# Performance work log

Measured on AMD Instinct MI355X. Metric: run time of the kernel, lower is better.

## Reference

```python
import jax, jax.numpy as jnp
import numpy as np

H = 1024
NH = 16
HD = H // NH
EPS = 1e-5


def setup_inputs() -> dict:
    key = jax.random.key(0)
    ks = jax.random.split(key, 16)
    B, LQ, LK = 2, 1024, 2048
    s = 1.0 / np.sqrt(H)
    inp = {
        "query": jax.random.normal(ks[0], (B, LQ, H), jnp.float32),
        "key": jax.random.normal(ks[1], (B, LK, H), jnp.float32),
        "value": jax.random.normal(ks[2], (B, LK, H), jnp.float32),
        "mask": jax.random.randint(ks[3], (B, LQ, LK), 0, 2, jnp.int32),
        "Wq": jax.random.normal(ks[4], (H, H), jnp.float32) * s,
        "bq": jnp.zeros((H,), jnp.float32),
        "Wk": jax.random.normal(ks[5], (H, H), jnp.float32) * s,
        "bk": jnp.zeros((H,), jnp.float32),
        "Wv": jax.random.normal(ks[6], (H, H), jnp.float32) * s,
        "bv": jnp.zeros((H,), jnp.float32),
        "Wo": jax.random.normal(ks[7], (H, H), jnp.float32) * s,
        "bo": jnp.zeros((H,), jnp.float32),
        "ln_g": jnp.ones((H,), jnp.float32),
        "ln_b": jnp.zeros((H,), jnp.float32),
    }
    return inp


def _split_heads(x, B, L):
    # [B, L, H] -> [B, NH, L, HD]
    return x.reshape(B, L, NH, HD).transpose(0, 2, 1, 3)


def reference(query, key, value, mask, Wq, bq, Wk, bk, Wv, bv, Wo, bo, ln_g, ln_b):
    B, LQ, _ = query.shape
    LK = key.shape[1]
    # projections (torch Linear: x @ W.T + b)
    Q = _split_heads(query @ Wq.T + bq, B, LQ)   # [B,NH,LQ,HD]
    K = _split_heads(key   @ Wk.T + bk, B, LK)   # [B,NH,LK,HD]
    V = _split_heads(value @ Wv.T + bv, B, LK)   # [B,NH,LK,HD]
    scores = jnp.einsum('bhqd,bhkd->bhqk', Q, K) / np.sqrt(HD)
    scores = jnp.where(mask[:, None, :, :] == 0, jnp.float32(-1e9), scores)
    attn = jax.nn.softmax(scores, axis=-1)
    # dropout is identity in eval mode
    ctx = jnp.einsum('bhqk,bhkd->bhqd', attn, V)            # [B,NH,LQ,HD]
    ctx = ctx.transpose(0, 2, 1, 3).reshape(B, LQ, H)       # [B,LQ,H]
    out = ctx @ Wo.T + bo
    x = out + query
    mu = jnp.mean(x, axis=-1, keepdims=True)
    var = jnp.mean(jnp.square(x - mu), axis=-1, keepdims=True)
    return (x - mu) / jnp.sqrt(var + EPS) * ln_g + ln_b
```

## Files before the change

### kernel.cpp

```cpp
#include <hip/hip_runtime.h>
#include <hip/hip_bf16.h>

typedef __hip_bfloat16 hbf16;

#define Hdim 1024
#define NHEAD 16
#define HDIM 64
#define BATCH 2
#define LQ 1024
#define LK 2048
#define LN_EPS 1e-5f

typedef __bf16 bfv8 __attribute__((ext_vector_type(8)));
typedef float floatx4 __attribute__((ext_vector_type(4)));
typedef union { bfv8 v; unsigned short s[8]; } bfu8;

#define GP 72

__device__ inline bfv8 cvt2(const float4 x, const float4 y) {
    bfv8 r = {(__bf16)x.x, (__bf16)x.y, (__bf16)x.z, (__bf16)x.w,
              (__bf16)y.x, (__bf16)y.y, (__bf16)y.z, (__bf16)y.w};
    return r;
}

__global__ __launch_bounds__(256, 2) void proj_qkv(
    const float* __restrict__ query, const float* __restrict__ key,
    const float* __restrict__ value,
    const float* __restrict__ Wq, const float* __restrict__ bq,
    const float* __restrict__ Wk, const float* __restrict__ bk,
    const float* __restrict__ Wv, const float* __restrict__ bv,
    hbf16* __restrict__ Qp, hbf16* __restrict__ Kp, hbf16* __restrict__ Vp) {
    const int z = blockIdx.z;
    if (z == 0 && blockIdx.y >= (BATCH * LQ) / 128) return;

    const float* A; const float* W; const float* bias; hbf16* out;
    if (z == 0)      { A = query; W = Wq; bias = bq; out = Qp; }
    else if (z == 1) { A = key;   W = Wk; bias = bk; out = Kp; }
    else             { A = value; W = Wv; bias = bv; out = Vp; }

    __shared__ __align__(16) __bf16 As[128 * GP];
    __shared__ __align__(16) __bf16 Bs[128 * GP];
    const int tid = threadIdx.x;
    const int lane = tid & 63;
    const int w = tid >> 6;
    const int wm = w & 1, wn = w >> 1;
    const int u = lane & 15, quad = lane >> 4;
    const int rowBase = blockIdx.y * 128;
    const int colBase = blockIdx.x * 128;
    const int srow = tid >> 3;
    const int scol = (tid & 7) * 8;

    floatx4 acc[4][4] = {};

    for (int k0 = 0; k0 < Hdim; k0 += 64) {
        bfv8 av[4], bv8[4];
#pragma unroll
        for (int p = 0; p < 4; ++p) {
            const float* ap = A + (size_t)(rowBase + p * 32 + srow) * Hdim + k0 + scol;
            av[p] = cvt2(((const float4*)ap)[0], ((const float4*)ap)[1]);
            const float* wp = W + (size_t)(colBase + p * 32 + srow) * Hdim + k0 + scol;
            bv8[p] = cvt2(((const float4*)wp)[0], ((const float4*)wp)[1]);
        }
        __syncthreads();
#pragma unroll
        for (int p = 0; p < 4; ++p) {
            *(bfv8*)&As[(p * 32 + srow) * GP + scol] = av[p];
            *(bfv8*)&Bs[(p * 32 + srow) * GP + scol] = bv8[p];
        }
        __syncthreads();
#pragma unroll
        for (int ks = 0; ks < 64; ks += 32) {
            bfv8 af[4], bf[4];
#pragma unroll
            for (int i = 0; i < 4; ++i) {
                af[i] = *(const bfv8*)&As[(wm * 64 + i * 16 + u) * GP + ks + quad * 8];
                bf[i] = *(const bfv8*)&Bs[(wn * 64 + i * 16 + u) * GP + ks + quad * 8];
            }
#pragma unroll
            for (int mt = 0; mt < 4; ++mt)
#pragma unroll
                for (int nt = 0; nt < 4; ++nt)
                    acc[mt][nt] = __builtin_amdgcn_mfma_f32_16x16x32_bf16(af[mt], bf[nt], acc[mt][nt], 0, 0, 0);
        }
    }

#pragma unroll
    for (int nt = 0; nt < 4; ++nt) {
        const int n = colBase + wn * 64 + nt * 16 + u;
        const float bn = bias[n];
#pragma unroll
        for (int mt = 0; mt < 4; ++mt)
#pragma unroll
            for (int rr = 0; rr < 4; ++rr) {
                const int m = rowBase + wm * 64 + mt * 16 + quad * 4 + rr;
                out[(size_t)m * Hdim + n] = __float2bfloat16(acc[mt][nt][rr] + bn);
            }
    }
}

__global__ __launch_bounds__(256, 2) void gemm_ctx128(const hbf16* __restrict__ A,
                                                      const float* __restrict__ W,
                                                      const float* __restrict__ bias,
                                                      const float* __restrict__ resid,
                                                      float* __restrict__ out) {
    __shared__ __align__(16) __bf16 As[128 * GP];
    __shared__ __align__(16) __bf16 Bs[128 * GP];
    const int tid = threadIdx.x;
    const int lane = tid & 63;
    const int w = tid >> 6;
    const int wm = w & 1, wn = w >> 1;
    const int u = lane & 15, quad = lane >> 4;
    const int rowBase = blockIdx.y * 128;
    const int colBase = blockIdx.x * 128;
    const int srow = tid >> 3;
    const int scol = (tid & 7) * 8;

    floatx4 acc[4][4] = {};

    for (int k0 = 0; k0 < Hdim; k0 += 64) {
        bfv8 av[4], bv8[4];
#pragma unroll
        for (int p = 0; p < 4; ++p) {
            av[p] = *(const bfv8*)(A + (size_t)(rowBase + p * 32 + srow) * Hdim + k0 + scol);
            const float* wp = W + (size_t)(colBase + p * 32 + srow) * Hdim + k0 + scol;
            bv8[p] = cvt2(((const float4*)wp)[0], ((const float4*)wp)[1]);
        }
        __syncthreads();
#pragma unroll
        for (int p = 0; p < 4; ++p) {
            *(bfv8*)&As[(p * 32 + srow) * GP + scol] = av[p];
            *(bfv8*)&Bs[(p * 32 + srow) * GP + scol] = bv8[p];
        }
        __syncthreads();
#pragma unroll
        for (int ks = 0; ks < 64; ks += 32) {
            bfv8 af[4], bf[4];
#pragma unroll
            for (int i = 0; i < 4; ++i) {
                af[i] = *(const bfv8*)&As[(wm * 64 + i * 16 + u) * GP + ks + quad * 8];
                bf[i] = *(const bfv8*)&Bs[(wn * 64 + i * 16 + u) * GP + ks + quad * 8];
            }
#pragma unroll
            for (int mt = 0; mt < 4; ++mt)
#pragma unroll
                for (int nt = 0; nt < 4; ++nt)
                    acc[mt][nt] = __builtin_amdgcn_mfma_f32_16x16x32_bf16(af[mt], bf[nt], acc[mt][nt], 0, 0, 0);
        }
    }

#pragma unroll
    for (int nt = 0; nt < 4; ++nt) {
        const int n = colBase + wn * 64 + nt * 16 + u;
        const float bn = bias[n];
#pragma unroll
        for (int mt = 0; mt < 4; ++mt)
#pragma unroll
            for (int rr = 0; rr < 4; ++rr) {
                const int m = rowBase + wm * 64 + mt * 16 + quad * 4 + rr;
                out[(size_t)m * Hdim + n] = acc[mt][nt][rr] + bn + resid[(size_t)m * Hdim + n];
            }
    }
}

#define QT 64
#define KT 64
#define KS_PITCH 72
#define VT_OFF(d) ((d) * 72 + (((d) >> 3) << 3))
#define PS_OFF(r) ((r) * 72 + (((r) >> 2) << 3))

__global__ __launch_bounds__(256, 4) void attn_flash(const hbf16* __restrict__ Qp,
                                                     const hbf16* __restrict__ Kp,
                                                     const hbf16* __restrict__ Vp,
                                                     const int* __restrict__ mask,
                                                     hbf16* __restrict__ ctx) {
    const int qb = blockIdx.x;
    const int h = blockIdx.y;
    const int b = blockIdx.z;
    const int tid = threadIdx.x;
    const int lane = tid & 63;
    const int w = tid >> 6;
    const int u = lane & 15;
    const int quad = lane >> 4;
    const int qBase = qb * QT;

    __shared__ __align__(16) __bf16 Ks[64 * KS_PITCH];
    __shared__ __align__(16) __bf16 Vt[4672];
    __shared__ __align__(16) __bf16 Ps[4][1184];

    const int qrow_frag = qBase + w * 16 + u;
    const hbf16* qptr = Qp + (size_t)(b * LQ + qrow_frag) * Hdim + h * HDIM + quad * 8;
    const bfv8 af_q0 = *(const bfv8*)qptr;
    const bfv8 af_q1 = *(const bfv8*)(qptr + 32);

    float m_run[4], l_run[4];
    floatx4 acc_o[4];
#pragma unroll
    for (int r = 0; r < 4; ++r) { m_run[r] = -1e30f; l_run[r] = 0.f; }
#pragma unroll
    for (int nd = 0; nd < 4; ++nd) acc_o[nd] = (floatx4){0.f, 0.f, 0.f, 0.f};

    const int sk = tid >> 2;
    const int sdg = (tid & 3) * 16;
    const int vk2 = (tid >> 3) * 2;
    const int vd0 = (tid & 7) * 8;
    const int* mbase = mask + ((size_t)(b * LQ + qBase + w * 16 + quad * 4)) * LK + u;

    for (int kt = 0; kt < LK / KT; ++kt) {
        const int kBase = kt * KT;

        int mv[4][4];
#pragma unroll
        for (int ns = 0; ns < 4; ++ns)
#pragma unroll
            for (int rr = 0; rr < 4; ++rr)
                mv[ns][rr] = mbase[(size_t)rr * LK + kBase + ns * 16];

        const hbf16* vp0 = Vp + (size_t)(b * LK + kBase + vk2) * Hdim + h * HDIM + vd0;
        bfu8 v0, v1;
        v0.v = *(const bfv8*)vp0;
        v1.v = *(const bfv8*)(vp0 + Hdim);
        const hbf16* kp = Kp + (size_t)(b * LK + kBase + sk) * Hdim + h * HDIM + sdg;
        const bfv8 kv0 = *(const bfv8*)kp;
        const bfv8 kv1 = *(const bfv8*)(kp + 8);

        __syncthreads();
        *(bfv8*)&Ks[sk * KS_PITCH + sdg] = kv0;
        *(bfv8*)&Ks[sk * KS_PITCH + sdg + 8] = kv1;
#pragma unroll
        for (int i = 0; i < 8; ++i) {
            unsigned int pk = (unsigned int)v0.s[i] | ((unsigned int)v1.s[i] << 16);
            *(unsigned int*)&Vt[VT_OFF(vd0 + i) + vk2] = pk;
        }
        __syncthreads();

        floatx4 acc_s[4];
#pragma unroll
        for (int ns = 0; ns < 4; ++ns) {
            const bfv8 bk0 = *(const bfv8*)&Ks[(ns * 16 + u) * KS_PITCH + quad * 8];
            const bfv8 bk1 = *(const bfv8*)&Ks[(ns * 16 + u) * KS_PITCH + quad * 8 + 32];
            floatx4 a = (floatx4){0.f, 0.f, 0.f, 0.f};
            a = __builtin_amdgcn_mfma_f32_16x16x32_bf16(af_q0, bk0, a, 0, 0, 0);
            a = __builtin_amdgcn_mfma_f32_16x16x32_bf16(af_q1, bk1, a, 0, 0, 0);
            acc_s[ns] = a;
        }

        float pvv[4][4];
#pragma unroll
        for (int ns = 0; ns < 4; ++ns)
#pragma unroll
            for (int rr = 0; rr < 4; ++rr) {
                float s = acc_s[ns][rr] * 0.125f;
                if (mv[ns][rr] == 0) s = -1e9f;
                pvv[ns][rr] = s;
            }

        float alpha[4];
#pragma unroll
        for (int rr = 0; rr < 4; ++rr) {
            float tmax = fmaxf(fmaxf(pvv[0][rr], pvv[1][rr]), fmaxf(pvv[2][rr], pvv[3][rr]));
            tmax = fmaxf(tmax, __shfl_xor(tmax, 1, 64));
            tmax = fmaxf(tmax, __shfl_xor(tmax, 2, 64));
            tmax = fmaxf(tmax, __shfl_xor(tmax, 4, 64));
            tmax = fmaxf(tmax, __shfl_xor(tmax, 8, 64));
            const float mn = fmaxf(m_run[rr], tmax);
            alpha[rr] = __expf(m_run[rr] - mn);
            m_run[rr] = mn;
            float tsum = 0.f;
#pragma unroll
            for (int ns = 0; ns < 4; ++ns) {
                const float e = __expf(pvv[ns][rr] - mn);
                pvv[ns][rr] = e;
                tsum += e;
            }
            tsum += __shfl_xor(tsum, 1, 64);
            tsum += __shfl_xor(tsum, 2, 64);
            tsum += __shfl_xor(tsum, 4, 64);
            tsum += __shfl_xor(tsum, 8, 64);
            l_run[rr] = l_run[rr] * alpha[rr] + tsum;
        }

        __bf16* Pw = Ps[w];
#pragma unroll
        for (int ns = 0; ns < 4; ++ns)
#pragma unroll
            for (int rr = 0; rr < 4; ++rr)
                Pw[PS_OFF(quad * 4 + rr) + ns * 16 + u] = (__bf16)pvv[ns][rr];
#pragma unroll
        for (int nd = 0; nd < 4; ++nd)
#pragma unroll
            for (int rr = 0; rr < 4; ++rr)
                acc_o[nd][rr] *= alpha[rr];

        const bfv8 af_p0 = *(const bfv8*)&Pw[PS_OFF(u) + quad * 8];
        const bfv8 af_p1 = *(const bfv8*)&Pw[PS_OFF(u) + quad * 8 + 32];
#pragma unroll
        for (int nd = 0; nd < 4; ++nd) {
            const bfv8 bv0 = *(const bfv8*)&Vt[VT_OFF(nd * 16 + u) + quad * 8];
            const bfv8 bv1 = *(const bfv8*)&Vt[VT_OFF(nd * 16 + u) + quad * 8 + 32];
            acc_o[nd] = __builtin_amdgcn_mfma_f32_16x16x32_bf16(af_p0, bv0, acc_o[nd], 0, 0, 0);
            acc_o[nd] = __builtin_amdgcn_mfma_f32_16x16x32_bf16(af_p1, bv1, acc_o[nd], 0, 0, 0);
        }
    }

#pragma unroll
    for (int rr = 0; rr < 4; ++rr) {
        const float invl = 1.0f / l_run[rr];
        const int qrow = qBase + w * 16 + quad * 4 + rr;
        hbf16* crow = ctx + (size_t)(b * LQ + qrow) * Hdim + h * HDIM;
#pragma unroll
        for (int nd = 0; nd < 4; ++nd)
            crow[nd * 16 + u] = __float2bfloat16(acc_o[nd][rr] * invl);
    }
}

__global__ __launch_bounds__(256) void ln_kernel(float* __restrict__ x,
                                                 const float* __restrict__ g,
                                                 const float* __restrict__ beta) {
    const int row = blockIdx.x;
    float* xr = x + (size_t)row * Hdim;
    __shared__ float red[256];
    const int tid = threadIdx.x;

    const float4 xi = ((const float4*)xr)[tid];
    red[tid] = xi.x + xi.y + xi.z + xi.w;
    __syncthreads();
    for (int st = 128; st > 0; st >>= 1) {
        if (tid < st) red[tid] += red[tid + st];
        __syncthreads();
    }
    const float mu = red[0] * (1.0f / Hdim);
    __syncthreads();
    {
        float dx = xi.x - mu, dy = xi.y - mu, dz = xi.z - mu, dw = xi.w - mu;
        red[tid] = dx * dx + dy * dy + dz * dz + dw * dw;
    }
    __syncthreads();
    for (int st = 128; st > 0; st >>= 1) {
        if (tid < st) red[tid] += red[tid + st];
        __syncthreads();
    }
    const float rstd = rsqrtf(red[0] * (1.0f / Hdim) + LN_EPS);

    const float4 g4 = ((const float4*)g)[tid];
    const float4 b4 = ((const float4*)beta)[tid];
    float4 y;
    y.x = (xi.x - mu) * rstd * g4.x + b4.x;
    y.y = (xi.y - mu) * rstd * g4.y + b4.y;
    y.z = (xi.z - mu) * rstd * g4.z + b4.z;
    y.w = (xi.w - mu) * rstd * g4.w + b4.w;
    ((float4*)xr)[tid] = y;
}

__device__ inline float wave_red_sum(float v) {
    v += __shfl_down(v, 32, 64);
    v += __shfl_down(v, 16, 64);
    v += __shfl_down(v, 8, 64);
    v += __shfl_down(v, 4, 64);
    v += __shfl_down(v, 2, 64);
    v += __shfl_down(v, 1, 64);
    return v;
}

__global__ __launch_bounds__(256) void fused_mha(
    const float* __restrict__ q_in, const float* __restrict__ k_in,
    const float* __restrict__ v_in, const int* __restrict__ mask,
    const float* __restrict__ Wq, const float* __restrict__ bq,
    const float* __restrict__ Wk, const float* __restrict__ bk,
    const float* __restrict__ Wv, const float* __restrict__ bv,
    const float* __restrict__ Wo, const float* __restrict__ bo,
    const float* __restrict__ ln_g, const float* __restrict__ ln_b,
    float* __restrict__ out) {
    const int q = blockIdx.x;
    const int b = blockIdx.y;
    const int tid = threadIdx.x;
    const int lane = tid & 63;
    const int w = tid >> 6;

    __shared__ float qrow[Hdim];
    __shared__ float qt[Hdim];
    __shared__ float sc[LK];
    __shared__ float u[Hdim];
    __shared__ float ctxv[Hdim];
    __shared__ float Qh[HDIM];
    __shared__ float red[256];
    __shared__ float sb_sh;

    const float* qp = q_in + (size_t)(b * LQ + q) * Hdim;
    for (int i = tid; i < Hdim; i += 256) qrow[i] = qp[i];
    __syncthreads();

    const float* keyb = k_in + (size_t)b * LK * Hdim;
    const float* valb = v_in + (size_t)b * LK * Hdim;
    const int* mrow = mask + (size_t)(b * LQ + q) * LK;

    for (int h = 0; h < NHEAD; ++h) {
        for (int dd = w; dd < HDIM; dd += 4) {
            const float4* wrow = (const float4*)(Wq + (size_t)(h * HDIM + dd) * Hdim);
            const float4* q4 = (const float4*)qrow;
            float p = 0.f;
#pragma unroll
            for (int i0 = 0; i0 < 4; ++i0) {
                float4 a = wrow[i0 * 64 + lane];
                float4 c = q4[i0 * 64 + lane];
                p += a.x * c.x + a.y * c.y + a.z * c.z + a.w * c.w;
            }
            p = wave_red_sum(p);
            if (lane == 0) Qh[dd] = p + bq[h * HDIM + dd];
        }
        __syncthreads();

        if (tid < HDIM) red[tid] = Qh[tid] * bk[h * HDIM + tid];

        float4 s4 = {0.f, 0.f, 0.f, 0.f};
        for (int d = 0; d < HDIM; ++d) {
            float4 a = ((const float4*)(Wk + (size_t)(h * HDIM + d) * Hdim))[tid];
            float qd = Qh[d];
            s4.x += a.x * qd;
            s4.y += a.y * qd;
            s4.z += a.z * qd;
            s4.w += a.w * qd;
        }
        __syncthreads();
        if (tid == 0) {
            float s = 0.f;
            for (int i = 0; i < HDIM; ++i) s += red[i];
            sb_sh = s;
        }
        ((float4*)qt)[tid] = s4;
        __syncthreads();
        const float sb = sb_sh;

        for (int k = w; k < LK; k += 4) {
            const float4* krow = (const float4*)(keyb + (size_t)k * Hdim);
            const float4* q4 = (const float4*)qt;
            float p = 0.f;
#pragma unroll
            for (int i0 = 0; i0 < 4; ++i0) {
                float4 a = krow[i0 * 64 + lane];
                float4 c = q4[i0 * 64 + lane];
                p += a.x * c.x + a.y * c.y + a.z * c.z + a.w * c.w;
            }
            p = wave_red_sum(p);
            if (lane == 0) {
                float s = (p + sb) * 0.125f;
                if (mrow[k] == 0) s = -1e9f;
                sc[k] = s;
            }
        }
        __syncthreads();

        float m = -1e30f;
        for (int k = tid; k < LK; k += 256) m = fmaxf(m, sc[k]);
        red[tid] = m;
        __syncthreads();
        for (int s = 128; s > 0; s >>= 1) {
            if (tid < s) red[tid] = fmaxf(red[tid], red[tid + s]);
            __syncthreads();
        }
        const float mx = red[0];
        __syncthreads();
        float sum = 0.f;
        for (int k = tid; k < LK; k += 256) {
            float e = __expf(sc[k] - mx);
            sc[k] = e;
            sum += e;
        }
        red[tid] = sum;
        __syncthreads();
        for (int s = 128; s > 0; s >>= 1) {
            if (tid < s) red[tid] += red[tid + s];
            __syncthreads();
        }
        const float inv = 1.0f / red[0];
        for (int k = tid; k < LK; k += 256) sc[k] *= inv;
        __syncthreads();

        {
            float4 acc = {0.f, 0.f, 0.f, 0.f};
            const float4* vb4 = (const float4*)valb;
#pragma unroll 4
            for (int k = 0; k < LK; ++k) {
                float p = sc[k];
                float4 a = vb4[(size_t)k * (Hdim / 4) + tid];
                acc.x += a.x * p;
                acc.y += a.y * p;
                acc.z += a.z * p;
                acc.w += a.w * p;
            }
            ((float4*)u)[tid] = acc;
        }
        __syncthreads();

        for (int dd = w; dd < HDIM; dd += 4) {
            const float4* wrow = (const float4*)(Wv + (size_t)(h * HDIM + dd) * Hdim);
            const float4* u4 = (const float4*)u;
            float p = 0.f;
#pragma unroll
            for (int i0 = 0; i0 < 4; ++i0) {
                float4 a = wrow[i0 * 64 + lane];
                float4 c = u4[i0 * 64 + lane];
                p += a.x * c.x + a.y * c.y + a.z * c.z + a.w * c.w;
            }
            p = wave_red_sum(p);
            if (lane == 0) ctxv[h * HDIM + dd] = p + bv[h * HDIM + dd];
        }
        __syncthreads();
    }

    for (int n = w; n < Hdim; n += 4) {
        const float4* wrow = (const float4*)(Wo + (size_t)n * Hdim);
        const float4* c4 = (const float4*)ctxv;
        float p = 0.f;
#pragma unroll
        for (int i0 = 0; i0 < 4; ++i0) {
            float4 a = wrow[i0 * 64 + lane];
            float4 c = c4[i0 * 64 + lane];
            p += a.x * c.x + a.y * c.y + a.z * c.z + a.w * c.w;
        }
        p = wave_red_sum(p);
        if (lane == 0) qt[n] = p + bo[n] + qrow[n];
    }
    __syncthreads();

    {
        const float4 x4 = ((const float4*)qt)[tid];
        red[tid] = x4.x + x4.y + x4.z + x4.w;
    }
    __syncthreads();
    for (int s = 128; s > 0; s >>= 1) {
        if (tid < s) red[tid] += red[tid + s];
        __syncthreads();
    }
    const float mu = red[0] * (1.0f / Hdim);
    __syncthreads();
    {
        const float4 x4 = ((const float4*)qt)[tid];
        float dx = x4.x - mu, dy = x4.y - mu, dz = x4.z - mu, dw = x4.w - mu;
        red[tid] = dx * dx + dy * dy + dz * dz + dw * dw;
    }
    __syncthreads();
    for (int s = 128; s > 0; s >>= 1) {
        if (tid < s) red[tid] += red[tid + s];
        __syncthreads();
    }
    const float rstd = rsqrtf(red[0] * (1.0f / Hdim) + LN_EPS);

    float* orow = out + (size_t)(b * LQ + q) * Hdim;
    const float4 x4 = ((const float4*)qt)[tid];
    const float4 g4 = ((const float4*)ln_g)[tid];
    const float4 b4 = ((const float4*)ln_b)[tid];
    float4 y;
    y.x = (x4.x - mu) * rstd * g4.x + b4.x;
    y.y = (x4.y - mu) * rstd * g4.y + b4.y;
    y.z = (x4.z - mu) * rstd * g4.z + b4.z;
    y.w = (x4.w - mu) * rstd * g4.w + b4.w;
    ((float4*)orow)[tid] = y;
}

extern "C" void kernel_launch(void* const* d_in, const int* in_sizes, int n_in,
                              void* d_out, int out_size, void* d_ws, size_t ws_size,
                              hipStream_t stream) {
    const float* query = (const float*)d_in[0];
    const float* key   = (const float*)d_in[1];
    const float* value = (const float*)d_in[2];
    const int*   mask  = (const int*)d_in[3];
    const float* Wq = (const float*)d_in[4];
    const float* bq = (const float*)d_in[5];
    const float* Wk = (const float*)d_in[6];
    const float* bk = (const float*)d_in[7];
    const float* Wv = (const float*)d_in[8];
    const float* bv = (const float*)d_in[9];
    const float* Wo = (const float*)d_in[10];
    const float* bo = (const float*)d_in[11];
    const float* ln_g = (const float*)d_in[12];
    const float* ln_b = (const float*)d_in[13];
    float* out = (float*)d_out;

    const size_t need = (size_t)(4 + 8 + 8 + 4) * 1024 * 1024;
    if (ws_size >= need) {
        char* p = (char*)d_ws;
        hbf16* Qp = (hbf16*)p;   p += (size_t)BATCH * LQ * Hdim * sizeof(hbf16);
        hbf16* Kp = (hbf16*)p;   p += (size_t)BATCH * LK * Hdim * sizeof(hbf16);
        hbf16* Vp = (hbf16*)p;   p += (size_t)BATCH * LK * Hdim * sizeof(hbf16);
        hbf16* ctxb = (hbf16*)p; p += (size_t)BATCH * LQ * Hdim * sizeof(hbf16);

        dim3 blk(256);
        proj_qkv<<<dim3(Hdim / 128, (BATCH * LK) / 128, 3), blk, 0, stream>>>(
            query, key, value, Wq, bq, Wk, bk, Wv, bv, Qp, Kp, Vp);

        attn_flash<<<dim3(LQ / QT, NHEAD, BATCH), blk, 0, stream>>>(Qp, Kp, Vp, mask, ctxb);

        gemm_ctx128<<<dim3(Hdim / 128, (BATCH * LQ) / 128), blk, 0, stream>>>(ctxb, Wo, bo, query, out);

        ln_kernel<<<BATCH * LQ, blk, 0, stream>>>(out, ln_g, ln_b);
    } else {
        fused_mha<<<dim3(LQ, BATCH), dim3(256), 0, stream>>>(
            query, key, value, mask, Wq, bq, Wk, bk, Wv, bv, Wo, bo, ln_g, ln_b, out);
    }
}
```

Measured before the change: 288.2 us.

## Pre-convert inputs and weights to bf16 and precompute mask bias in fragment layout

Adds a conversion pass that casts activations and all four weight matrices to bf16, so the projection and output GEMMs load bf16 directly instead of converting fp32 in the inner loop. A mask_prep kernel turns the int32 mask into a bf16 additive bias, stored in the MFMA fragment order so attention reads one bf16 vector per tile instead of scattered int loads. The 1/sqrt(d) scale is folded into the Q projection. This costs extra kernel launches and an extra read and write pass over inputs, the mask and the weights, plus roughly 60MB of workspace. The old path remains as a fallback when the workspace is too small.

```diff
diff --git a/kernel.cpp b/kernel.cpp
--- a/kernel.cpp
+++ b/kernel.cpp
@@ -13,7 +13,7 @@
 
 typedef __bf16 bfv8 __attribute__((ext_vector_type(8)));
 typedef float floatx4 __attribute__((ext_vector_type(4)));
-typedef union { bfv8 v; unsigned short s[8]; } bfu8;
+typedef union { bfv8 v; __bf16 b[8]; unsigned short s[8]; } bfu8;
 
 #define GP 72
 
@@ -21,6 +21,344 @@
     bfv8 r = {(__bf16)x.x, (__bf16)x.y, (__bf16)x.z, (__bf16)x.w,
               (__bf16)y.x, (__bf16)y.y, (__bf16)y.z, (__bf16)y.w};
     return r;
+}
+
+__global__ __launch_bounds__(256) void cvt_bf16_multi(
+    const float* __restrict__ q, const float* __restrict__ k, const float* __restrict__ v,
+    const float* __restrict__ Wq, const float* __restrict__ Wk,
+    const float* __restrict__ Wv, const float* __restrict__ Wo,
+    hbf16* __restrict__ dq, hbf16* __restrict__ dk, hbf16* __restrict__ dv,
+    hbf16* __restrict__ dWq, hbf16* __restrict__ dWk,
+    hbf16* __restrict__ dWv, hbf16* __restrict__ dWo) {
+    const int z = blockIdx.z;
+    const float* src; hbf16* dst; int n;
+    switch (z) {
+        case 0: src = q;  dst = dq;  n = BATCH * LQ * Hdim; break;
+        case 1: src = k;  dst = dk;  n = BATCH * LK * Hdim; break;
+        case 2: src = v;  dst = dv;  n = BATCH * LK * Hdim; break;
+        case 3: src = Wq; dst = dWq; n = Hdim * Hdim; break;
+        case 4: src = Wk; dst = dWk; n = Hdim * Hdim; break;
+        case 5: src = Wv; dst = dWv; n = Hdim * Hdim; break;
+        default: src = Wo; dst = dWo; n = Hdim * Hdim; break;
+    }
+    const int idx = (blockIdx.x * 256 + threadIdx.x) * 8;
+    if (idx >= n) return;
+    const float4 a = ((const float4*)(src + idx))[0];
+    const float4 b = ((const float4*)(src + idx))[1];
+    *(bfv8*)(dst + idx) = cvt2(a, b);
+}
+
+__global__ __launch_bounds__(256) void mask_prep(const int* __restrict__ mask,
+                                                 hbf16* __restrict__ mbias) {
+    const int t = blockIdx.x;
+    const int kt = t & 31;
+    const int qb = (t >> 5) & 15;
+    const int b = t >> 9;
+    const int tid = threadIdx.x;
+    const int w = tid >> 6;
+    const int lane = tid & 63;
+    const int quad = lane >> 4;
+    const int u = lane & 15;
+    const int qrow = qb * 64 + w * 16 + quad * 4;
+    const int kcol = kt * 64 + u;
+    const int* mp = mask + ((size_t)(b * LQ + qrow)) * LK + kcol;
+
+    bfu8 v0, v1;
+#pragma unroll
+    for (int ns = 0; ns < 4; ++ns)
+#pragma unroll
+        for (int rr = 0; rr < 4; ++rr) {
+            const int mv = mp[(size_t)rr * LK + ns * 16];
+            const __bf16 bias = (mv == 0) ? (__bf16)(-1e9f) : (__bf16)0.0f;
+            const int j = ns * 4 + rr;
+            if (j < 8) v0.b[j] = bias; else v1.b[j - 8] = bias;
+        }
+    __bf16* dst = (__bf16*)mbias + (size_t)t * 4096 + tid * 16;
+    *(bfv8*)dst = v0.v;
+    *(bfv8*)(dst + 8) = v1.v;
+}
+
+__global__ __launch_bounds__(256, 2) void proj_qkv_bf(
+    const hbf16* __restrict__ xq, const hbf16* __restrict__ xk, const hbf16* __restrict__ xv,
+    const hbf16* __restrict__ Wq, const float* __restrict__ bq,
+    const hbf16* __restrict__ Wk, const float* __restrict__ bk,
+    const hbf16* __restrict__ Wv, const float* __restrict__ bv,
+    hbf16* __restrict__ Qp, hbf16* __restrict__ Kp, hbf16* __restrict__ Vp) {
+    const int z = blockIdx.z;
+    if (z == 0 && blockIdx.y >= (BATCH * LQ) / 128) return;
+
+    const hbf16* A; const hbf16* W; const float* bias; hbf16* out; float scale;
+    if (z == 0)      { A = xq; W = Wq; bias = bq; out = Qp; scale = 0.125f; }
+    else if (z == 1) { A = xk; W = Wk; bias = bk; out = Kp; scale = 1.0f; }
+    else             { A = xv; W = Wv; bias = bv; out = Vp; scale = 1.0f; }
+
+    __shared__ __align__(16) __bf16 As[128 * GP];
+    __shared__ __align__(16) __bf16 Bs[128 * GP];
+    const int tid = threadIdx.x;
+    const int lane = tid & 63;
+    const int w = tid >> 6;
+    const int wm = w & 1, wn = w >> 1;
+    const int u = lane & 15, quad = lane >> 4;
+    const int rowBase = blockIdx.y * 128;
+    const int colBase = blockIdx.x * 128;
+    const int srow = tid >> 3;
+    const int scol = (tid & 7) * 8;
+
+    floatx4 acc[4][4] = {};
+
+    for (int k0 = 0; k0 < Hdim; k0 += 64) {
+        bfv8 av[4], bv8[4];
+#pragma unroll
+        for (int p = 0; p < 4; ++p) {
+            av[p] = *(const bfv8*)(A + (size_t)(rowBase + p * 32 + srow) * Hdim + k0 + scol);
+            bv8[p] = *(const bfv8*)(W + (size_t)(colBase + p * 32 + srow) * Hdim + k0 + scol);
+        }
+        __syncthreads();
+#pragma unroll
+        for (int p = 0; p < 4; ++p) {
+            *(bfv8*)&As[(p * 32 + srow) * GP + scol] = av[p];
+            *(bfv8*)&Bs[(p * 32 + srow) * GP + scol] = bv8[p];
+        }
+        __syncthreads();
+#pragma unroll
+        for (int ks = 0; ks < 64; ks += 32) {
+            bfv8 af[4], bf[4];
+#pragma unroll
+            for (int i = 0; i < 4; ++i) {
+                af[i] = *(const bfv8*)&As[(wm * 64 + i * 16 + u) * GP + ks + quad * 8];
+                bf[i] = *(const bfv8*)&Bs[(wn * 64 + i * 16 + u) * GP + ks + quad * 8];
+            }
+#pragma unroll
+            for (int mt = 0; mt < 4; ++mt)
+#pragma unroll
+                for (int nt = 0; nt < 4; ++nt)
+                    acc[mt][nt] = __builtin_amdgcn_mfma_f32_16x16x32_bf16(af[mt], bf[nt], acc[mt][nt], 0, 0, 0);
+        }
+    }
+
+#pragma unroll
+    for (int nt = 0; nt < 4; ++nt) {
+        const int n = colBase + wn * 64 + nt * 16 + u;
+        const float bn = bias[n];
+#pragma unroll
+        for (int mt = 0; mt < 4; ++mt)
+#pragma unroll
+            for (int rr = 0; rr < 4; ++rr) {
+                const int m = rowBase + wm * 64 + mt * 16 + quad * 4 + rr;
+                out[(size_t)m * Hdim + n] = __float2bfloat16((acc[mt][nt][rr] + bn) * scale);
+            }
+    }
+}
+
+__global__ __launch_bounds__(256, 2) void gemm_ctx_bf(const hbf16* __restrict__ A,
+                                                      const hbf16* __restrict__ W,
+                                                      const float* __restrict__ bias,
+                                                      const float* __restrict__ resid,
+                                                      float* __restrict__ out) {
+    __shared__ __align__(16) __bf16 As[128 * GP];
+    __shared__ __align__(16) __bf16 Bs[128 * GP];
+    const int tid = threadIdx.x;
+    const int lane = tid & 63;
+    const int w = tid >> 6;
+    const int wm = w & 1, wn = w >> 1;
+    const int u = lane & 15, quad = lane >> 4;
+    const int rowBase = blockIdx.y * 128;
+    const int colBase = blockIdx.x * 128;
+    const int srow = tid >> 3;
+    const int scol = (tid & 7) * 8;
+
+    floatx4 acc[4][4] = {};
+
+    for (int k0 = 0; k0 < Hdim; k0 += 64) {
+        bfv8 av[4], bv8[4];
+#pragma unroll
+        for (int p = 0; p < 4; ++p) {
+            av[p] = *(const bfv8*)(A + (size_t)(rowBase + p * 32 + srow) * Hdim + k0 + scol);
+            bv8[p] = *(const bfv8*)(W + (size_t)(colBase + p * 32 + srow) * Hdim + k0 + scol);
+        }
+        __syncthreads();
+#pragma unroll
+        for (int p = 0; p < 4; ++p) {
+            *(bfv8*)&As[(p * 32 + srow) * GP + scol] = av[p];
+            *(bfv8*)&Bs[(p * 32 + srow) * GP + scol] = bv8[p];
+        }
+        __syncthreads();
+#pragma unroll
+        for (int ks = 0; ks < 64; ks += 32) {
+            bfv8 af[4], bf[4];
+#pragma unroll
+            for (int i = 0; i < 4; ++i) {
+                af[i] = *(const bfv8*)&As[(wm * 64 + i * 16 + u) * GP + ks + quad * 8];
+                bf[i] = *(const bfv8*)&Bs[(wn * 64 + i * 16 + u) * GP + ks + quad * 8];
+            }
+#pragma unroll
+            for (int mt = 0; mt < 4; ++mt)
+#pragma unroll
+                for (int nt = 0; nt < 4; ++nt)
+                    acc[mt][nt] = __builtin_amdgcn_mfma_f32_16x16x32_bf16(af[mt], bf[nt], acc[mt][nt], 0, 0, 0);
+        }
+    }
+
+#pragma unroll
+    for (int nt = 0; nt < 4; ++nt) {
+        const int n = colBase + wn * 64 + nt * 16 + u;
+        const float bn = bias[n];
+#pragma unroll
+        for (int mt = 0; mt < 4; ++mt)
+#pragma unroll
+            for (int rr = 0; rr < 4; ++rr) {
+                const int m = rowBase + wm * 64 + mt * 16 + quad * 4 + rr;
+                out[(size_t)m * Hdim + n] = acc[mt][nt][rr] + bn + resid[(size_t)m * Hdim + n];
+            }
+    }
+}
+
+#define QT 64
+#define KT 64
+#define KS_PITCH 72
+#define VT_OFF(d) ((d) * 72 + (((d) >> 3) << 3))
+#define PS_OFF(r) ((r) * 72 + (((r) >> 2) << 3))
+
+__global__ __launch_bounds__(256, 4) void attn_flash_mb(const hbf16* __restrict__ Qp,
+                                                        const hbf16* __restrict__ Kp,
+                                                        const hbf16* __restrict__ Vp,
+                                                        const hbf16* __restrict__ mbias,
+                                                        hbf16* __restrict__ ctx) {
+    const int qb = blockIdx.x;
+    const int h = blockIdx.y;
+    const int b = blockIdx.z;
+    const int tid = threadIdx.x;
+    const int lane = tid & 63;
+    const int w = tid >> 6;
+    const int u = lane & 15;
+    const int quad = lane >> 4;
+    const int qBase = qb * QT;
+
+    __shared__ __align__(16) __bf16 Ks[64 * KS_PITCH];
+    __shared__ __align__(16) __bf16 Vt[4672];
+    __shared__ __align__(16) __bf16 Ps[4][1184];
+
+    const int qrow_frag = qBase + w * 16 + u;
+    const hbf16* qptr = Qp + (size_t)(b * LQ + qrow_frag) * Hdim + h * HDIM + quad * 8;
+    const bfv8 af_q0 = *(const bfv8*)qptr;
+    const bfv8 af_q1 = *(const bfv8*)(qptr + 32);
+
+    float m_run[4], l_run[4];
+    floatx4 acc_o[4];
+#pragma unroll
+    for (int r = 0; r < 4; ++r) { m_run[r] = -1e30f; l_run[r] = 0.f; }
+#pragma unroll
+    for (int nd = 0; nd < 4; ++nd) acc_o[nd] = (floatx4){0.f, 0.f, 0.f, 0.f};
+
+    const int sk = tid >> 2;
+    const int sdg = (tid & 3) * 16;
+    const int vk2 = (tid >> 3) * 2;
+    const int vd0 = (tid & 7) * 8;
+    const __bf16* mbT = (const __bf16*)mbias + (size_t)(b * 16 + qb) * 32 * 4096 + tid * 16;
+
+    for (int kt = 0; kt < LK / KT; ++kt) {
+        const int kBase = kt * KT;
+
+        bfu8 mb0, mb1;
+        mb0.v = *(const bfv8*)(mbT + (size_t)kt * 4096);
+        mb1.v = *(const bfv8*)(mbT + (size_t)kt * 4096 + 8);
+
+        const hbf16* vp0 = Vp + (size_t)(b * LK + kBase + vk2) * Hdim + h * HDIM + vd0;
+        bfu8 v0, v1;
+        v0.v = *(const bfv8*)vp0;
+        v1.v = *(const bfv8*)(vp0 + Hdim);
+        const hbf16* kp = Kp + (size_t)(b * LK + kBase + sk) * Hdim + h * HDIM + sdg;
+        const bfv8 kv0 = *(const bfv8*)kp;
+        const bfv8 kv1 = *(const bfv8*)(kp + 8);
+
+        __syncthreads();
+        *(bfv8*)&Ks[sk * KS_PITCH + sdg] = kv0;
+        *(bfv8*)&Ks[sk * KS_PITCH + sdg + 8] = kv1;
+#pragma unroll
+        for (int i = 0; i < 8; ++i) {
+            unsigned int pk = (unsigned int)v0.s[i] | ((unsigned int)v1.s[i] << 16);
+            *(unsigned int*)&Vt[VT_OFF(vd0 + i) + vk2] = pk;
+        }
+        __syncthreads();
+
+        floatx4 acc_s[4];
+#pragma unroll
+        for (int ns = 0; ns < 4; ++ns) {
+            const bfv8 bk0 = *(const bfv8*)&Ks[(ns * 16 + u) * KS_PITCH + quad * 8];
+            const bfv8 bk1 = *(const bfv8*)&Ks[(ns * 16 + u) * KS_PITCH + quad * 8 + 32];
+            floatx4 a = (floatx4){0.f, 0.f, 0.f, 0.f};
+            a = __builtin_amdgcn_mfma_f32_16x16x32_bf16(af_q0, bk0, a, 0, 0, 0);
+            a = __builtin_amdgcn_mfma_f32_16x16x32_bf16(af_q1, bk1, a, 0, 0, 0);
+            acc_s[ns] = a;
+        }
+
+        float pvv[4][4];
+#pragma unroll
+        for (int ns = 0; ns < 4; ++ns)
+#pragma unroll
+            for (int rr = 0; rr < 4; ++rr) {
+                const int j = ns * 4 + rr;
+                const float bias = (j < 8) ? (float)mb0.b[j] : (float)mb1.b[j - 8];
+                pvv[ns][rr] = acc_s[ns][rr] + bias;
+            }
+
+        float alpha[4];
+#pragma unroll
+        for (int rr = 0; rr < 4; ++rr) {
+            float tmax = fmaxf(fmaxf(pvv[0][rr], pvv[1][rr]), fmaxf(pvv[2][rr], pvv[3][rr]));
+            tmax = fmaxf(tmax, __shfl_xor(tmax, 1, 64));
+            tmax = fmaxf(tmax, __shfl_xor(tmax, 2, 64));
+            tmax = fmaxf(tmax, __shfl_xor(tmax, 4, 64));
+            tmax = fmaxf(tmax, __shfl_xor(tmax, 8, 64));
+            const float mn = fmaxf(m_run[rr], tmax);
+            alpha[rr] = __expf(m_run[rr] - mn);
+            m_run[rr] = mn;
+            float tsum = 0.f;
+#pragma unroll
+            for (int ns = 0; ns < 4; ++ns) {
+                const float e = __expf(pvv[ns][rr] - mn);
+                pvv[ns][rr] = e;
+                tsum += e;
+            }
+            tsum += __shfl_xor(tsum, 1, 64);
+            tsum += __shfl_xor(tsum, 2, 64);
+            tsum += __shfl_xor(tsum, 4, 64);
+            tsum += __shfl_xor(tsum, 8, 64);
+            l_run[rr] = l_run[rr] * alpha[rr] + tsum;
+        }
+
+        __bf16* Pw = Ps[w];
+#pragma unroll
+        for (int ns = 0; ns < 4; ++ns)
+#pragma unroll
+            for (int rr = 0; rr < 4; ++rr)
+                Pw[PS_OFF(quad * 4 + rr) + ns * 16 + u] = (__bf16)pvv[ns][rr];
+#pragma unroll
+        for (int nd = 0; nd < 4; ++nd)
+#pragma unroll
+            for (int rr = 0; rr < 4; ++rr)
+                acc_o[nd][rr] *= alpha[rr];
+
+        const bfv8 af_p0 = *(const bfv8*)&Pw[PS_OFF(u) + quad * 8];
+        const bfv8 af_p1 = *(const bfv8*)&Pw[PS_OFF(u) + quad * 8 + 32];
+#pragma unroll
+        for (int nd = 0; nd < 4; ++nd) {
+            const bfv8 bv0 = *(const bfv8*)&Vt[VT_OFF(nd * 16 + u) + quad * 8];
+            const bfv8 bv1 = *(const bfv8*)&Vt[VT_OFF(nd * 16 + u) + quad * 8 + 32];
+            acc_o[nd] = __builtin_amdgcn_mfma_f32_16x16x32_bf16(af_p0, bv0, acc_o[nd], 0, 0, 0);
+            acc_o[nd] = __builtin_amdgcn_mfma_f32_16x16x32_bf16(af_p1, bv1, acc_o[nd], 0, 0, 0);
+        }
+    }
+
+#pragma unroll
+    for (int rr = 0; rr < 4; ++rr) {
+        const float invl = 1.0f / l_run[rr];
+        const int qrow = qBase + w * 16 + quad * 4 + rr;
+        hbf16* crow = ctx + (size_t)(b * LQ + qrow) * Hdim + h * HDIM;
+#pragma unroll
+        for (int nd = 0; nd < 4; ++nd)
+            crow[nd * 16 + u] = __float2bfloat16(acc_o[nd][rr] * invl);
+    }
 }
 
 __global__ __launch_bounds__(256, 2) void proj_qkv(
@@ -161,12 +499,6 @@
             }
     }
 }
-
-#define QT 64
-#define KT 64
-#define KS_PITCH 72
-#define VT_OFF(d) ((d) * 72 + (((d) >> 3) << 3))
-#define PS_OFF(r) ((r) * 72 + (((r) >> 2) << 3))
 
 __global__ __launch_bounds__(256, 4) void attn_flash(const hbf16* __restrict__ Qp,
                                                      const hbf16* __restrict__ Kp,
@@ -576,22 +908,50 @@
     const float* ln_b = (const float*)d_in[13];
     float* out = (float*)d_out;
 
-    const size_t need = (size_t)(4 + 8 + 8 + 4) * 1024 * 1024;
-    if (ws_size >= need) {
+    const size_t MB = 1024 * 1024;
+    const size_t need_new = 60 * MB;
+    const size_t need_old = 24 * MB;
+    dim3 blk(256);
+
+    if (ws_size >= need_new) {
         char* p = (char*)d_ws;
-        hbf16* Qp = (hbf16*)p;   p += (size_t)BATCH * LQ * Hdim * sizeof(hbf16);
-        hbf16* Kp = (hbf16*)p;   p += (size_t)BATCH * LK * Hdim * sizeof(hbf16);
-        hbf16* Vp = (hbf16*)p;   p += (size_t)BATCH * LK * Hdim * sizeof(hbf16);
-        hbf16* ctxb = (hbf16*)p; p += (size_t)BATCH * LQ * Hdim * sizeof(hbf16);
-
-        dim3 blk(256);
+        hbf16* Qp = (hbf16*)p;    p += 4 * MB;
+        hbf16* Kp = (hbf16*)p;    p += 8 * MB;
+        hbf16* Vp = (hbf16*)p;    p += 8 * MB;
+        hbf16* ctxb = (hbf16*)p;  p += 4 * MB;
+        hbf16* xq16 = (hbf16*)p;  p += 4 * MB;
+        hbf16* xk16 = (hbf16*)p;  p += 8 * MB;
+        hbf16* xv16 = (hbf16*)p;  p += 8 * MB;
+        hbf16* Wq16 = (hbf16*)p;  p += 2 * MB;
+        hbf16* Wk16 = (hbf16*)p;  p += 2 * MB;
+        hbf16* Wv16 = (hbf16*)p;  p += 2 * MB;
+        hbf16* Wo16 = (hbf16*)p;  p += 2 * MB;
+        hbf16* mbias = (hbf16*)p; p += 8 * MB;
+
+        cvt_bf16_multi<<<dim3(2048, 1, 7), blk, 0, stream>>>(
+            query, key, value, Wq, Wk, Wv, Wo,
+            xq16, xk16, xv16, Wq16, Wk16, Wv16, Wo16);
+        mask_prep<<<dim3(1024), blk, 0, stream>>>(mask, mbias);
+
+        proj_qkv_bf<<<dim3(Hdim / 128, (BATCH * LK) / 128, 3), blk, 0, stream>>>(
+            xq16, xk16, xv16, Wq16, bq, Wk16, bk, Wv16, bv, Qp, Kp, Vp);
+
+        attn_flash_mb<<<dim3(LQ / QT, NHEAD, BATCH), blk, 0, stream>>>(Qp, Kp, Vp, mbias, ctxb);
+
+        gemm_ctx_bf<<<dim3(Hdim / 128, (BATCH * LQ) / 128), blk, 0, stream>>>(ctxb, Wo16, bo, query, out);
+
+        ln_kernel<<<BATCH * LQ, blk, 0, stream>>>(out, ln_g, ln_b);
+    } else if (ws_size >= need_old) {
+        char* p = (char*)d_ws;
+        hbf16* Qp = (hbf16*)p;   p += 4 * MB;
+        hbf16* Kp = (hbf16*)p;   p += 8 * MB;
+        hbf16* Vp = (hbf16*)p;   p += 8 * MB;
+        hbf16* ctxb = (hbf16*)p; p += 4 * MB;
+
         proj_qkv<<<dim3(Hdim / 128, (BATCH * LK) / 128, 3), blk, 0, stream>>>(
             query, key, value, Wq, bq, Wk, bk, Wv, bv, Qp, Kp, Vp);
-
         attn_flash<<<dim3(LQ / QT, NHEAD, BATCH), blk, 0, stream>>>(Qp, Kp, Vp, mask, ctxb);
-
         gemm_ctx128<<<dim3(Hdim / 128, (BATCH * LQ) / 128), blk, 0, stream>>>(ctxb, Wo, bo, query, out);
-
         ln_kernel<<<BATCH * LQ, blk, 0, stream>>>(out, ln_g, ln_b);
     } else {
         fused_mha<<<dim3(LQ, BATCH), dim3(256), 0, stream>>>(
```

Measured after the change: 276.2 us. 1.04x faster.
